# Kernel tuning notes

Hardware: AMD Instinct MI355X
Metric: run time of the kernel (lower is better)

Reference implementation:

```python
import jax, jax.numpy as jnp
import numpy as np

B, T, D = 1, 8192, 1024
H, DH = 16, 64
WIN = 128          # attention window (tokens on each side)
WB = 128
NB = T // WB
EPS = 1e-5


def _layernorm(x, g, b):
    mu = jnp.mean(x, axis=-1, keepdims=True)
    var = jnp.mean(jnp.square(x - mu), axis=-1, keepdims=True)
    return (x - mu) * jax.lax.rsqrt(var + EPS) * g + b


def _band_mask():
    # query offset i in [0, WB), key offset j in [0, 3*WB) within [prev|self|next] blocks
    i = jnp.arange(WB)[:, None]
    j = jnp.arange(3 * WB)[None, :]
    rel = j - WB - i                      # key_pos - query_pos
    band = jnp.abs(rel) <= WIN            # sliding window |i-j| <= W (matches torch mask)
    blk = jnp.arange(NB)[:, None, None]
    key_pos = blk * WB + (j - WB)[None]   # absolute key position
    return band[None] & (key_pos >= 0) & (key_pos < T)   # [NB, WB, 3*WB]


def _local_attention(q, k, v):
    # q,k,v: [B,H,T,DH] -> block-local SDPA, mathematically identical to
    # full SDPA with the additive band mask in the torch code.
    def blocks(t):
        return t.reshape(B, H, NB, WB, DH)
    qb = blocks(q)
    kp = jnp.pad(blocks(k), ((0, 0), (0, 0), (1, 1), (0, 0), (0, 0)))
    vp = jnp.pad(blocks(v), ((0, 0), (0, 0), (1, 1), (0, 0), (0, 0)))
    # gather [prev, self, next] key/value blocks: [B,H,NB,3*WB,DH]
    k3 = jnp.concatenate([kp[:, :, s:s + NB] for s in range(3)], axis=3)
    v3 = jnp.concatenate([vp[:, :, s:s + NB] for s in range(3)], axis=3)
    scores = jnp.einsum('bhnqd,bhnkd->bhnqk', qb, k3) / np.sqrt(DH).astype(np.float32)
    mask = _band_mask()                                   # [NB,WB,3WB]
    scores = jnp.where(mask[None, None], scores, -jnp.inf)
    attn = jax.nn.softmax(scores, axis=-1)
    out = jnp.einsum('bhnqk,bhnkd->bhnqd', attn, v3)      # [B,H,NB,WB,DH]
    return out.reshape(B, H, T, DH)


def setup_inputs() -> dict:
    key = jax.random.key(0)
    ks = jax.random.split(key, 7)
    s = 0.02
    return {
        'x': jax.random.normal(ks[0], (B, T, D), jnp.float32),
        'wq': jax.random.normal(ks[1], (D, D), jnp.float32) * s,
        'wk': jax.random.normal(ks[2], (D, D), jnp.float32) * s,
        'wv': jax.random.normal(ks[3], (D, D), jnp.float32) * s,
        'wo': jax.random.normal(ks[4], (D, D), jnp.float32) * s,
        'wg': jax.random.normal(ks[5], (D, 2 * D), jnp.float32) * s,
        'wd': jax.random.normal(ks[6], (2 * D, D), jnp.float32) * s,
        'norm_g': jnp.ones((D,), jnp.float32),
        'norm_b': jnp.zeros((D,), jnp.float32),
        'ffn_g': jnp.ones((D,), jnp.float32),
        'ffn_b': jnp.zeros((D,), jnp.float32),
    }


def reference(x, wq, wk, wv, wo, wg, wd, norm_g, norm_b, ffn_g, ffn_b):
    h = _layernorm(x, norm_g, norm_b)
    def heads(t):  # [B,T,D] -> [B,H,T,DH]
        return t.reshape(B, T, H, DH).transpose(0, 2, 1, 3)
    q, k, v = heads(h @ wq), heads(h @ wk), heads(h @ wv)
    attn_out = _local_attention(q, k, v)                     # [B,H,T,DH]
    attn_out = attn_out.transpose(0, 2, 1, 3).reshape(B, T, D)
    x = x + attn_out @ wo
    h = _layernorm(x, ffn_g, ffn_b)
    x = x + jax.nn.silu(h @ wg) @ wd
    return x
```

## Files before the change

kernel.cpp:

```cpp
#include <hip/hip_runtime.h>
#include <cstdint>

#define T_DIM 8192
#define D_DIM 1024
#define NB_DIM 64
#define QKS 2048

typedef __bf16 bf16x8 __attribute__((ext_vector_type(8)));
typedef __bf16 bf16x4 __attribute__((ext_vector_type(4)));
typedef float f32x4 __attribute__((ext_vector_type(4)));

#define MFMA16(a, b, c) __builtin_amdgcn_mfma_f32_16x16x32_bf16((a), (b), (c), 0, 0, 0)
#define BAR() asm volatile("s_barrier" ::: "memory")
#define LGK0()                                          \
  asm volatile("s_waitcnt lgkmcnt(0)" ::: "memory");    \
  __builtin_amdgcn_sched_barrier(0)
#define VMCNT(n) asm volatile("s_waitcnt vmcnt(" #n ")" ::: "memory")

__device__ __forceinline__ void gld_lds16(const void* gsrc, void* ldst) {
  __builtin_amdgcn_global_load_lds(
      (__attribute__((address_space(1))) void*)(uintptr_t)gsrc,
      (__attribute__((address_space(3))) void*)(uintptr_t)ldst,
      16, 0, 0);
}

__global__ __launch_bounds__(256) void transpose_cvt(
    const float* __restrict__ W, __bf16* __restrict__ Wt, int K, int N) {
  __shared__ float tile[32][33];
  const int tx = threadIdx.x & 31, ty = threadIdx.x >> 5;
  const int n0 = blockIdx.x * 32, k0 = blockIdx.y * 32;
#pragma unroll
  for (int i = 0; i < 32; i += 8)
    tile[ty + i][tx] = W[(size_t)(k0 + ty + i) * N + n0 + tx];
  __syncthreads();
#pragma unroll
  for (int i = 0; i < 32; i += 8)
    Wt[(size_t)(n0 + ty + i) * K + k0 + tx] = (__bf16)tile[tx][ty + i];
}

template <typename TI>
__global__ __launch_bounds__(256) void ln_kernel(
    const TI* __restrict__ x, const float* __restrict__ g,
    const float* __restrict__ b, __bf16* __restrict__ out) {
  __shared__ float red[8];
  const int row = blockIdx.x, tid = threadIdx.x;
  float v0, v1, v2, v3;
  if constexpr (sizeof(TI) == 4) {
    const float4 v = ((const float4*)(x + (size_t)row * D_DIM))[tid];
    v0 = v.x; v1 = v.y; v2 = v.z; v3 = v.w;
  } else {
    const bf16x4 v = ((const bf16x4*)(x + (size_t)row * D_DIM))[tid];
    v0 = (float)v[0]; v1 = (float)v[1]; v2 = (float)v[2]; v3 = (float)v[3];
  }
  float s = v0 + v1 + v2 + v3;
#pragma unroll
  for (int off = 32; off >= 1; off >>= 1) s += __shfl_xor(s, off, 64);
  if ((tid & 63) == 0) red[tid >> 6] = s;
  __syncthreads();
  const float mean = (red[0] + red[1] + red[2] + red[3]) * (1.0f / D_DIM);
  const float d0 = v0 - mean, d1 = v1 - mean, d2 = v2 - mean, d3 = v3 - mean;
  float ss = d0 * d0 + d1 * d1 + d2 * d2 + d3 * d3;
#pragma unroll
  for (int off = 32; off >= 1; off >>= 1) ss += __shfl_xor(ss, off, 64);
  if ((tid & 63) == 0) red[4 + (tid >> 6)] = ss;
  __syncthreads();
  const float var = (red[4] + red[5] + red[6] + red[7]) * (1.0f / D_DIM);
  const float rstd = rsqrtf(var + 1e-5f);
  const float4 gg = ((const float4*)g)[tid];
  const float4 bb = ((const float4*)b)[tid];
  bf16x4 o;
  o[0] = (__bf16)(d0 * rstd * gg.x + bb.x);
  o[1] = (__bf16)(d1 * rstd * gg.y + bb.y);
  o[2] = (__bf16)(d2 * rstd * gg.z + bb.z);
  o[3] = (__bf16)(d3 * rstd * gg.w + bb.w);
  *(bf16x4*)(out + (size_t)row * D_DIM + tid * 4) = o;
}

__global__ __launch_bounds__(256, 2) void gemm_vt(
    const __bf16* __restrict__ A, const __bf16* __restrict__ Bt,
    __bf16* __restrict__ Cout, int M, int N, int K) {
  __shared__ __bf16 smem[32768];
  __bf16* As = smem;
  __bf16* Bs = smem + 16384;
  const int tid = threadIdx.x;
  const int l = tid & 63, w = tid >> 6;
  const int lr = l & 15, lg = l >> 4;
  const int wr = w >> 1, wc = w & 1;
  const int bm = blockIdx.y, bn = blockIdx.x;
  const size_t arow0 = (size_t)bm * 128;
  const size_t brow0 = (size_t)bn * 128;

  f32x4 acc[4][4];
  const f32x4 z4 = {0.f, 0.f, 0.f, 0.f};
#pragma unroll
  for (int m = 0; m < 4; ++m)
#pragma unroll
    for (int n = 0; n < 4; ++n) acc[m][n] = z4;

  auto stage = [&](int buf, int k0) {
#pragma unroll
    for (int r = 0; r < 4; ++r) {
      int ci = r * 256 + tid;
      int row = ci >> 3, c8 = ci & 7;
      gld_lds16(A + (arow0 + row) * K + k0 + c8 * 8, &As[buf * 8192 + ci * 8]);
    }
#pragma unroll
    for (int r = 0; r < 4; ++r) {
      int ci = r * 256 + tid;
      int row = ci >> 3, c8 = ci & 7;
      gld_lds16(Bt + (brow0 + row) * K + k0 + c8 * 8, &Bs[buf * 8192 + ci * 8]);
    }
  };

  stage(0, 0);
  const int nk = K >> 6;
  int cur = 0;
  __syncthreads();

  for (int t = 0; t < nk; ++t) {
    if (t + 1 < nk) stage(cur ^ 1, (t + 1) << 6);
#pragma unroll
    for (int kk = 0; kk < 2; ++kk) {
      bf16x8 af[4], bf_[4];
#pragma unroll
      for (int m = 0; m < 4; ++m)
        af[m] = *(const bf16x8*)&As[cur * 8192 + (wr * 64 + m * 16 + lr) * 64 + kk * 32 + lg * 8];
#pragma unroll
      for (int n = 0; n < 4; ++n)
        bf_[n] = *(const bf16x8*)&Bs[cur * 8192 + (wc * 64 + n * 16 + lr) * 64 + kk * 32 + lg * 8];
#pragma unroll
      for (int m = 0; m < 4; ++m)
#pragma unroll
        for (int n = 0; n < 4; ++n) acc[m][n] = MFMA16(af[m], bf_[n], acc[m][n]);
    }
    __syncthreads();
    cur ^= 1;
  }

  __bf16* Tt = smem;
#pragma unroll
  for (int m = 0; m < 4; ++m)
#pragma unroll
    for (int n = 0; n < 4; ++n)
#pragma unroll
      for (int r = 0; r < 4; ++r)
        Tt[(wc * 64 + n * 16 + lr) * 136 + wr * 64 + m * 16 + lg * 4 + r] =
            (__bf16)acc[m][n][r];
  __syncthreads();
#pragma unroll
  for (int i = 0; i < 8; ++i) {
    const int ci = i * 256 + tid;
    const int c = ci >> 4;
    const int rr = (ci & 15) * 8;
    const bf16x8 vv = *(const bf16x8*)&Tt[c * 136 + rr];
    *(bf16x8*)(Cout + (size_t)(bn * 128 + c) * M + bm * 128 + rr) = vv;
  }
}

template <int BM_, int EPI>
__global__ __launch_bounds__(512, 2) void gemm8(
    const __bf16* __restrict__ A, const __bf16* __restrict__ Bt,
    const void* __restrict__ Res, void* __restrict__ Cout,
    int M, int N, int K, int nbn) {
  constexpr int MF = BM_ / 32;
  constexpr int MH = MF / 2;
  constexpr int SA = 8 * MF;
  constexpr int LA = BM_ / 128;
  constexpr int ATILE = BM_ * 64;
  constexpr int AHALF = BM_ * 32;
  constexpr int BOFF = 2 * ATILE;
  __shared__ __bf16 lds[2 * BM_ * 64 + 32768];

  const int tid = threadIdx.x;
  const int l = tid & 63, w = tid >> 6;
  const int lr = l & 15, lg = l >> 4;
  const int wr = w >> 2, wc = w & 3;
  const int nwg = gridDim.x;
  const int bid = (int)blockIdx.x;
  const int swz = (bid & 7) * (nwg >> 3) + (bid >> 3);
  const int bm = swz / nbn, bn = swz % nbn;
  const int am0 = bm * BM_, bn0 = bn * 256;

  f32x4 acc[MF][4];
  const f32x4 z4 = {0.f, 0.f, 0.f, 0.f};
#pragma unroll
  for (int m = 0; m < MF; ++m)
#pragma unroll
    for (int n = 0; n < 4; ++n) acc[m][n] = z4;

  auto stageA = [&](int h, int b, int k0) {
#pragma unroll
    for (int r = 0; r < LA; ++r) {
      const int ci = r * 512 + tid;
      const int wri = ci >> 3, c8 = ci & 7;
      const int ra = (wri % SA) + (wri / SA) * (2 * SA) + h * SA;
      gld_lds16(A + (size_t)(am0 + ra) * K + k0 + ((c8 ^ (wri & 7)) << 3),
                (__bf16*)lds + b * ATILE + h * AHALF + ci * 8);
    }
  };
  auto stageB = [&](int h, int b, int k0) {
#pragma unroll
    for (int r = 0; r < 2; ++r) {
      const int ci = r * 512 + tid;
      const int wri = ci >> 3, c8 = ci & 7;
      const int rb = (wri & 31) + (wri >> 5) * 64 + h * 32;
      gld_lds16(Bt + (size_t)(bn0 + rb) * K + k0 + ((c8 ^ (wri & 7)) << 3),
                (__bf16*)lds + BOFF + b * 16384 + h * 8192 + ci * 8);
    }
  };

  int buf = 0;
  auto lda = [&](int mh, int i, int kk) -> bf16x8 {
    const int rl = (i * 16 + lr) + wr * SA;
    const int ch = (kk * 4 + lg) ^ (rl & 7);
    return *(const bf16x8*)&lds[buf * ATILE + mh * AHALF + rl * 64 + ch * 8];
  };
  auto ldb = [&](int nh, int j, int kk) -> bf16x8 {
    const int rl = (j * 16 + lr) + wc * 32;
    const int ch = (kk * 4 + lg) ^ (rl & 7);
    return *(const bf16x8*)&lds[BOFF + buf * 16384 + nh * 8192 + rl * 64 + ch * 8];
  };

  const int nt = K >> 6;
  stageA(0, 0, 0);
  stageB(0, 0, 0);
  stageB(1, 0, 0);
  stageA(1, 0, 0);
  if constexpr (BM_ == 256) VMCNT(4); else VMCNT(3);
  BAR();

  bf16x8 afr[MH][2], bfr[2][2];
  for (int t = 0; t < nt; ++t) {
    const int nb = buf ^ 1;
    const int kn = (t + 1) << 6;
    const bool st = (t + 1 < nt);

#pragma unroll
    for (int i = 0; i < MH; ++i)
#pragma unroll
      for (int kk = 0; kk < 2; ++kk) afr[i][kk] = lda(0, i, kk);
#pragma unroll
    for (int j = 0; j < 2; ++j)
#pragma unroll
      for (int kk = 0; kk < 2; ++kk) bfr[j][kk] = ldb(0, j, kk);
    if (st) {
      stageA(0, nb, kn);
      if constexpr (BM_ == 256) VMCNT(4); else VMCNT(2);
    } else {
      if constexpr (BM_ == 256) VMCNT(2); else VMCNT(1);
    }
    BAR();
    LGK0();
    __builtin_amdgcn_s_setprio(1);
#pragma unroll
    for (int i = 0; i < MH; ++i)
#pragma unroll
      for (int j = 0; j < 2; ++j)
#pragma unroll
        for (int kk = 0; kk < 2; ++kk)
          acc[i][j] = MFMA16(afr[i][kk], bfr[j][kk], acc[i][j]);
    __builtin_amdgcn_sched_barrier(0);
    __builtin_amdgcn_s_setprio(0);
    BAR();

#pragma unroll
    for (int j = 0; j < 2; ++j)
#pragma unroll
      for (int kk = 0; kk < 2; ++kk) bfr[j][kk] = ldb(1, j, kk);
    if (st) {
      stageB(0, nb, kn);
      if constexpr (BM_ == 256) VMCNT(4); else VMCNT(3);
    } else {
      VMCNT(0);
    }
    BAR();
    LGK0();
    __builtin_amdgcn_s_setprio(1);
#pragma unroll
    for (int i = 0; i < MH; ++i)
#pragma unroll
      for (int j = 0; j < 2; ++j)
#pragma unroll
        for (int kk = 0; kk < 2; ++kk)
          acc[i][2 + j] = MFMA16(afr[i][kk], bfr[j][kk], acc[i][2 + j]);
    __builtin_amdgcn_sched_barrier(0);
    __builtin_amdgcn_s_setprio(0);
    BAR();

#pragma unroll
    for (int i = 0; i < MH; ++i)
#pragma unroll
      for (int kk = 0; kk < 2; ++kk) afr[i][kk] = lda(1, i, kk);
    if (st) stageB(1, nb, kn);
    BAR();
    LGK0();
    __builtin_amdgcn_s_setprio(1);
#pragma unroll
    for (int i = 0; i < MH; ++i)
#pragma unroll
      for (int j = 0; j < 2; ++j)
#pragma unroll
        for (int kk = 0; kk < 2; ++kk)
          acc[MH + i][2 + j] = MFMA16(afr[i][kk], bfr[j][kk], acc[MH + i][2 + j]);
    __builtin_amdgcn_sched_barrier(0);
    __builtin_amdgcn_s_setprio(0);
    BAR();

#pragma unroll
    for (int j = 0; j < 2; ++j)
#pragma unroll
      for (int kk = 0; kk < 2; ++kk) bfr[j][kk] = ldb(0, j, kk);
    if (st) {
      stageA(1, nb, kn);
      if constexpr (BM_ == 256) VMCNT(4); else VMCNT(3);
    }
    BAR();
    LGK0();
    __builtin_amdgcn_s_setprio(1);
#pragma unroll
    for (int i = 0; i < MH; ++i)
#pragma unroll
      for (int j = 0; j < 2; ++j)
#pragma unroll
        for (int kk = 0; kk < 2; ++kk)
          acc[MH + i][j] = MFMA16(afr[i][kk], bfr[j][kk], acc[MH + i][j]);
    __builtin_amdgcn_sched_barrier(0);
    __builtin_amdgcn_s_setprio(0);
    BAR();

    buf = nb;
  }

  if constexpr (EPI == 5) {
    const __bf16* R = (const __bf16*)Res;
    float* O = (float*)Cout;
#pragma unroll
    for (int mf = 0; mf < MF; ++mf)
#pragma unroll
      for (int nf = 0; nf < 4; ++nf)
#pragma unroll
        for (int r = 0; r < 4; ++r) {
          const int row = am0 + wr * 2 * SA + mf * 16 + lg * 4 + r;
          const int col = bn0 + wc * 64 + nf * 16 + lr;
          const size_t idx = (size_t)row * N + col;
          O[idx] = acc[mf][nf][r] + (float)R[idx];
        }
  } else {
    __bf16* Ct = (__bf16*)lds;
#pragma unroll
    for (int mf = 0; mf < MF; ++mf)
#pragma unroll
      for (int nf = 0; nf < 4; ++nf)
#pragma unroll
        for (int r = 0; r < 4; ++r) {
          const int rl = wr * 2 * SA + mf * 16 + lg * 4 + r;
          const int cl = wc * 64 + nf * 16 + lr;
          float v = acc[mf][nf][r];
          if constexpr (EPI == 3) v = v / (1.f + __expf(-v));
          if constexpr (EPI == 4)
            v += ((const float*)Res)[(size_t)(am0 + rl) * N + bn0 + cl];
          Ct[rl * 256 + cl] = (__bf16)v;
        }
    __syncthreads();
    __bf16* O = (__bf16*)Cout;
#pragma unroll
    for (int i = 0; i < BM_ / 16; ++i) {
      const int ci = i * 512 + tid;
      const int row = ci >> 5, c8 = ci & 31;
      *(bf16x8*)(O + (size_t)(am0 + row) * N + bn0 + c8 * 8) =
          *(const bf16x8*)&Ct[row * 256 + c8 * 8];
    }
  }
}

__global__ __launch_bounds__(256, 2) void attn_kernel(
    const __bf16* __restrict__ qk, const __bf16* __restrict__ vT,
    __bf16* __restrict__ out) {
  __shared__ __bf16 Pl[4][32 * 136];

  const int tid = threadIdx.x;
  const int l = tid & 63, w = tid >> 6;
  const int lr = l & 15, lg = l >> 4;
  const int bx = (int)blockIdx.x;
  const int swz = (bx & 7) * 128 + (bx >> 3);
  const int h = swz >> 6;
  const int blk = swz & 63;
  __bf16* Pw = Pl[w];

  const __bf16* qbase =
      qk + (size_t)(blk * 128 + w * 32 + lr) * QKS + h * 64 + lg * 8;
  bf16x8 qf[2][2];
#pragma unroll
  for (int m = 0; m < 2; ++m)
#pragma unroll
    for (int ks = 0; ks < 2; ++ks)
      qf[m][ks] = *(const bf16x8*)(qbase + (size_t)m * 16 * QKS + ks * 32);

  const f32x4 z4 = {0.f, 0.f, 0.f, 0.f};
  float ssum[2][4];
  f32x4 o[2][4];
#pragma unroll
  for (int m = 0; m < 2; ++m) {
#pragma unroll
    for (int r = 0; r < 4; ++r) ssum[m][r] = 0.f;
#pragma unroll
    for (int n = 0; n < 4; ++n) o[m][n] = z4;
  }

  for (int it = 0; it < 3; ++it) {
    const int kb = blk + it - 1;
    if (kb < 0 || kb >= NB_DIM) continue;
    const int rel = it - 1;
    const int kclo = (rel < 0) ? (w * 2) : 0;
    const int kchi = (rel > 0) ? (w * 2 + 2) : 8;

    f32x4 s[2][8];
    const __bf16* kbase =
        qk + (size_t)(kb * 128 + lr) * QKS + 1024 + h * 64 + lg * 8;
#pragma unroll
    for (int kc = 0; kc < 8; ++kc) {
      if (kc < kclo || kc >= kchi) continue;
      const bf16x8 k0 = *(const bf16x8*)(kbase + (size_t)kc * 16 * QKS);
      const bf16x8 k1 = *(const bf16x8*)(kbase + (size_t)kc * 16 * QKS + 32);
      s[0][kc] = MFMA16(qf[0][0], k0, z4);
      s[1][kc] = MFMA16(qf[1][0], k0, z4);
      s[0][kc] = MFMA16(qf[0][1], k1, s[0][kc]);
      s[1][kc] = MFMA16(qf[1][1], k1, s[1][kc]);
    }

#pragma unroll
    for (int m = 0; m < 2; ++m) {
#pragma unroll
      for (int r = 0; r < 4; ++r) {
        const int qi = w * 32 + m * 16 + lg * 4 + r;
        float acc_s = 0.f;
#pragma unroll
        for (int kc = 0; kc < 8; ++kc) {
          if (kc < kclo || kc >= kchi) continue;
          const int kj = kc * 16 + lr;
          float p = __expf(s[m][kc][r] * 0.125f);
          const bool valid = (rel == 0) || (rel < 0 ? (kj >= qi) : (kj <= qi));
          p = valid ? p : 0.f;
          s[m][kc][r] = p;
          acc_s += p;
        }
        ssum[m][r] += acc_s;
      }
    }

#pragma unroll
    for (int m = 0; m < 2; ++m)
#pragma unroll
      for (int kc = 0; kc < 8; ++kc) {
        if (kc < kclo || kc >= kchi) continue;
#pragma unroll
        for (int r = 0; r < 4; ++r)
          Pw[(m * 16 + lg * 4 + r) * 136 + kc * 16 + lr] = (__bf16)s[m][kc][r];
      }

    const int kslo = kclo >> 1, kshi = kchi >> 1;
    const __bf16* vbase =
        vT + (size_t)(h * 64 + lr) * T_DIM + kb * 128 + lg * 8;
#pragma unroll
    for (int ks = 0; ks < 4; ++ks) {
      if (ks < kslo || ks >= kshi) continue;
      bf16x8 pa[2];
#pragma unroll
      for (int m = 0; m < 2; ++m)
        pa[m] = *(const bf16x8*)&Pw[(m * 16 + lr) * 136 + ks * 32 + lg * 8];
#pragma unroll
      for (int n = 0; n < 4; ++n) {
        const bf16x8 vb = *(const bf16x8*)(vbase + (size_t)n * 16 * T_DIM + ks * 32);
        o[0][n] = MFMA16(pa[0], vb, o[0][n]);
        o[1][n] = MFMA16(pa[1], vb, o[1][n]);
      }
    }
  }

  float inv[2][4];
#pragma unroll
  for (int m = 0; m < 2; ++m)
#pragma unroll
    for (int r = 0; r < 4; ++r) {
      float rs = ssum[m][r];
#pragma unroll
      for (int off = 1; off < 16; off <<= 1) rs += __shfl_xor(rs, off, 64);
      inv[m][r] = __builtin_amdgcn_rcpf(rs);
    }
#pragma unroll
  for (int m = 0; m < 2; ++m)
#pragma unroll
    for (int n = 0; n < 4; ++n)
#pragma unroll
      for (int r = 0; r < 4; ++r)
        Pw[(m * 16 + lg * 4 + r) * 136 + n * 16 + lr] =
            (__bf16)(o[m][n][r] * inv[m][r]);
#pragma unroll
  for (int i = 0; i < 4; ++i) {
    const int ci = i * 64 + l;
    const int qrow = ci >> 3;
    const int c8 = (ci & 7) * 8;
    const bf16x8 vv = *(const bf16x8*)&Pw[qrow * 136 + c8];
    *(bf16x8*)(out + (size_t)(blk * 128 + w * 32 + qrow) * D_DIM + h * 64 + c8) = vv;
  }
}

extern "C" void kernel_launch(void* const* d_in, const int* in_sizes, int n_in,
                              void* d_out, int out_size, void* d_ws, size_t ws_size,
                              hipStream_t stream) {
  (void)in_sizes; (void)n_in; (void)out_size; (void)ws_size;
  const float* x      = (const float*)d_in[0];
  const float* wq     = (const float*)d_in[1];
  const float* wk     = (const float*)d_in[2];
  const float* wv     = (const float*)d_in[3];
  const float* wo     = (const float*)d_in[4];
  const float* wg     = (const float*)d_in[5];
  const float* wd     = (const float*)d_in[6];
  const float* norm_g = (const float*)d_in[7];
  const float* norm_b = (const float*)d_in[8];
  const float* ffn_g  = (const float*)d_in[9];
  const float* ffn_b  = (const float*)d_in[10];
  float* out = (float*)d_out;

  char* ws = (char*)d_ws;
  constexpr size_t MB = 1ull << 20;
  __bf16* wqkT = (__bf16*)(ws + 0 * MB);
  __bf16* wvT  = (__bf16*)(ws + 4 * MB);
  __bf16* woT  = (__bf16*)(ws + 6 * MB);
  __bf16* wgT  = (__bf16*)(ws + 8 * MB);
  __bf16* wdT  = (__bf16*)(ws + 12 * MB);
  __bf16* hbuf = (__bf16*)(ws + 16 * MB);
  __bf16* qkbf = (__bf16*)(ws + 32 * MB);
  __bf16* gbf  = (__bf16*)(ws + 32 * MB);
  __bf16* vTbf = (__bf16*)(ws + 64 * MB);
  __bf16* x2bf = (__bf16*)(ws + 80 * MB);

  transpose_cvt<<<dim3(32, 32), 256, 0, stream>>>(wq, wqkT, 1024, 1024);
  transpose_cvt<<<dim3(32, 32), 256, 0, stream>>>(wk, wqkT + 1024 * 1024, 1024, 1024);
  transpose_cvt<<<dim3(32, 32), 256, 0, stream>>>(wv, wvT, 1024, 1024);
  transpose_cvt<<<dim3(32, 32), 256, 0, stream>>>(wo, woT, 1024, 1024);
  transpose_cvt<<<dim3(64, 32), 256, 0, stream>>>(wg, wgT, 1024, 2048);
  transpose_cvt<<<dim3(32, 64), 256, 0, stream>>>(wd, wdT, 2048, 1024);

  ln_kernel<float><<<8192, 256, 0, stream>>>(x, norm_g, norm_b, hbuf);

  gemm8<256, 0><<<256, 512, 0, stream>>>(hbuf, wqkT, nullptr, qkbf, 8192, 2048, 1024, 8);
  gemm_vt<<<dim3(8, 64), 256, 0, stream>>>(hbuf, wvT, vTbf, 8192, 1024, 1024);

  attn_kernel<<<1024, 256, 0, stream>>>(qkbf, vTbf, hbuf);

  gemm8<128, 4><<<256, 512, 0, stream>>>(hbuf, woT, x, x2bf, 8192, 1024, 1024, 4);

  ln_kernel<__bf16><<<8192, 256, 0, stream>>>(x2bf, ffn_g, ffn_b, hbuf);

  gemm8<256, 3><<<256, 512, 0, stream>>>(hbuf, wgT, nullptr, gbf, 8192, 2048, 1024, 8);

  gemm8<128, 5><<<256, 512, 0, stream>>>(gbf, wdT, x2bf, out, 8192, 1024, 2048, 4);
}
```

Baseline: 269.2 us.

## Deepen GEMM global-to-LDS prefetch to stage half-tiles two iterations ahead

```diff
diff --git a/kernel.cpp b/kernel.cpp
--- a/kernel.cpp
+++ b/kernel.cpp
@@ -223,17 +223,21 @@
 
   const int nt = K >> 6;
   stageA(0, 0, 0);
+  stageB(1, 0, 0);
   stageB(0, 0, 0);
-  stageB(1, 0, 0);
   stageA(1, 0, 0);
-  if constexpr (BM_ == 256) VMCNT(4); else VMCNT(3);
+  stageA(0, 1, 64);
+  stageB(1, 1, 64);
+  if constexpr (BM_ == 256) VMCNT(6); else VMCNT(4);
   BAR();
 
   bf16x8 afr[MH][2], bfr[2][2];
   for (int t = 0; t < nt; ++t) {
-    const int nb = buf ^ 1;
-    const int kn = (t + 1) << 6;
-    const bool st = (t + 1 < nt);
+    const bool s1 = (t + 1 < nt);
+    const bool s2 = (t + 2 < nt);
+    const int b1 = (t + 1) & 1;
+    const int k1 = (t + 1) << 6;
+    const int k2 = (t + 2) << 6;
 
 #pragma unroll
     for (int i = 0; i < MH; ++i)
@@ -243,12 +247,7 @@
     for (int j = 0; j < 2; ++j)
 #pragma unroll
       for (int kk = 0; kk < 2; ++kk) bfr[j][kk] = ldb(0, j, kk);
-    if (st) {
-      stageA(0, nb, kn);
-      if constexpr (BM_ == 256) VMCNT(4); else VMCNT(2);
-    } else {
-      if constexpr (BM_ == 256) VMCNT(2); else VMCNT(1);
-    }
+    if (s1) stageB(0, b1, k1);
     BAR();
     LGK0();
     __builtin_amdgcn_s_setprio(1);
@@ -267,11 +266,9 @@
     for (int j = 0; j < 2; ++j)
 #pragma unroll
       for (int kk = 0; kk < 2; ++kk) bfr[j][kk] = ldb(1, j, kk);
-    if (st) {
-      stageB(0, nb, kn);
-      if constexpr (BM_ == 256) VMCNT(4); else VMCNT(3);
-    } else {
-      VMCNT(0);
+    if (s1) {
+      stageA(1, b1, k1);
+      if constexpr (BM_ == 256) VMCNT(8); else VMCNT(6);
     }
     BAR();
     LGK0();
@@ -291,7 +288,7 @@
     for (int i = 0; i < MH; ++i)
 #pragma unroll
       for (int kk = 0; kk < 2; ++kk) afr[i][kk] = lda(1, i, kk);
-    if (st) stageB(1, nb, kn);
+    if (s2) stageA(0, buf, k2);
     BAR();
     LGK0();
     __builtin_amdgcn_s_setprio(1);
@@ -310,9 +307,11 @@
     for (int j = 0; j < 2; ++j)
 #pragma unroll
       for (int kk = 0; kk < 2; ++kk) bfr[j][kk] = ldb(0, j, kk);
-    if (st) {
-      stageA(1, nb, kn);
-      if constexpr (BM_ == 256) VMCNT(4); else VMCNT(3);
+    if (s2) {
+      stageB(1, buf, k2);
+      if constexpr (BM_ == 256) VMCNT(6); else VMCNT(4);
+    } else if (s1) {
+      VMCNT(0);
     }
     BAR();
     LGK0();
@@ -328,7 +327,7 @@
     __builtin_amdgcn_s_setprio(0);
     BAR();
 
-    buf = nb;
+    buf ^= 1;
   }
 
   if constexpr (EPI == 5) {
```

After: 266.4 us. Within noise of the previous version (-1.0%).
